# Kernel optimization log

Hardware: AMD Instinct MI355X
Metric: run time of the kernel (lower is better)

The kernel has to match this reference:

```python
import jax, jax.numpy as jnp
import numpy as np

B, S, T = 64, 1024, 64
H, A, DA, DT, P, NT = 1024, 1024, 512, 256, 256, 32
DIN = DA + A + DT  # LSTMCell input: [a_tm1_embed, att_tm1, pre_type]


def setup_inputs() -> dict:
    key = jax.random.key(0)
    ks = jax.random.split(key, 16)
    nrm = lambda k, shape, s=0.02: jax.random.normal(k, shape, jnp.float32) * s
    return {
        'src_encodings': jax.random.normal(ks[0], (B, S, H), jnp.float32),
        'W_ih': nrm(ks[1], (4 * H, DIN)), 'b_ih': jnp.zeros((4 * H,), jnp.float32),
        'W_hh': nrm(ks[2], (4 * H, H)), 'b_hh': jnp.zeros((4 * H,), jnp.float32),
        'W_att': nrm(ks[3], (H, H)),            # att_sketch_linear (no bias)
        'W_attvec': nrm(ks[4], (A, 2 * H)),     # sketch_att_vec_linear (no bias)
        'W_init': nrm(ks[5], (H, H)), 'b_init': jnp.zeros((H,), jnp.float32),  # decoder_cell_init
        'W_q2a': nrm(ks[6], (DA, A)), 'b_q2a': jnp.zeros((DA,), jnp.float32),  # query_vec_to_action_embed
        'prod_embed': nrm(ks[7], (P, DA), 0.05), 'prod_bias': jnp.zeros((P,), jnp.float32),
        'type_embed': nrm(ks[8], (NT, DT), 0.05),
        'prev_prod_ids': jax.random.randint(ks[9], (B, T), 0, P),
        'prev_type_ids': jax.random.randint(ks[10], (B, T), 0, NT),
        'target_prod_ids': jax.random.randint(ks[11], (B, T), 0, P),
        'sketch_lens': jax.random.randint(ks[12], (B,), T // 2, T + 1),
        'src_lens': jax.random.randint(ks[13], (B,), S // 2, S + 1),
    }


def _lstm_cell(x, h, c, W_ih, b_ih, W_hh, b_hh):
    gates = x @ W_ih.T + b_ih + h @ W_hh.T + b_hh
    i, f, g, o = jnp.split(gates, 4, axis=-1)
    c_new = jax.nn.sigmoid(f) * c + jax.nn.sigmoid(i) * jnp.tanh(g)
    h_new = jax.nn.sigmoid(o) * jnp.tanh(c_new)
    return h_new, c_new


def reference(src_encodings, W_ih, b_ih, W_hh, b_hh, W_att, W_attvec, W_init, b_init,
              W_q2a, b_q2a, prod_embed, prod_bias, type_embed,
              prev_prod_ids, prev_type_ids, target_prod_ids, sketch_lens, src_lens):
    Bq, Sq, Hq = src_encodings.shape
    Tq = prev_prod_ids.shape[1]
    src_valid = jnp.arange(Sq)[None, :] < src_lens[:, None]            # [B,S] True = real token
    step_valid = jnp.arange(Tq)[None, :] < sketch_lens[:, None]        # [B,T]
    prev_valid = step_valid & (jnp.arange(Tq)[None, :] > 0)            # prev action exists

    src_att = jnp.einsum('bsh,kh->bsk', src_encodings, W_att)          # att_sketch_linear
    # init_decoder_state(adaptive_avg_pool1d(enc,1))
    init_cell = src_encodings.mean(axis=1)
    h0 = jnp.tanh(init_cell @ W_init.T + b_init)
    c0 = jnp.zeros_like(h0)
    att0 = jnp.zeros((Bq, A), src_encodings.dtype)

    # precomputed grammar lookups (production / type embeddings of a_{t-1})
    a_embeds = jnp.where(prev_valid[..., None], prod_embed[prev_prod_ids], 0.0)   # [B,T,DA]
    t_embeds = jnp.where(prev_valid[..., None], type_embed[prev_type_ids], 0.0)   # [B,T,DT]
    is_first = jnp.arange(Tq) == 0                                                # [T]

    def step(carry, inp):
        h, c, att_tm1 = carry
        a_e, t_e, first = inp
        x = jnp.concatenate([a_e, att_tm1, t_e], axis=-1)
        x = jnp.where(first, 0.0, x)                                   # t==0 -> zero input
        h, c = _lstm_cell(x, h, c, W_ih, b_ih, W_hh, b_hh)
        scores = jnp.einsum('bh,bsh->bs', h, src_att)
        scores = jnp.where(src_valid, scores, -1e9)
        alpha = jax.nn.softmax(scores, axis=-1)
        ctx = jnp.einsum('bs,bsh->bh', alpha, src_encodings)
        att_t = jnp.tanh(jnp.concatenate([h, ctx], axis=-1) @ W_attvec.T)
        q = jnp.tanh(att_t @ W_q2a.T + b_q2a)                          # non_linear readout
        probs = jax.nn.softmax(q @ prod_embed.T + prod_bias, axis=-1)  # [B,P]
        return (h, c, att_t), probs

    xs = (jnp.swapaxes(a_embeds, 0, 1), jnp.swapaxes(t_embeds, 0, 1), is_first)
    _, probs = jax.lax.scan(step, (h0, c0, att0), xs)                  # [T,B,P]

    tgt = jnp.swapaxes(target_prod_ids, 0, 1)[..., None]               # [T,B,1]
    p_t = jnp.take_along_axis(probs, tgt, axis=-1)[..., 0]             # [T,B]
    logp = jnp.log(p_t + 1e-8)
    sketch_prob = jnp.sum(jnp.where(step_valid.T, logp, 0.0), axis=0)  # [B]
    return sketch_prob
```

## Files before the change

### kernel.cpp

```cpp
#include <hip/hip_runtime.h>
#include <hip/hip_bf16.h>

typedef unsigned short u16;
typedef unsigned int u32;
typedef unsigned long long u64;
typedef __attribute__((ext_vector_type(8))) short short8;
typedef __attribute__((ext_vector_type(8))) u16 ushort8;
typedef __attribute__((ext_vector_type(4))) u16 ushort4v;
typedef __attribute__((ext_vector_type(4))) float f32x4;

__device__ __forceinline__ float bf2f(u16 x){ u32 u=((u32)x)<<16; return __builtin_bit_cast(float,u); }
__device__ __forceinline__ u16 f2bf(float f){ u32 u=__builtin_bit_cast(u32,f); u32 r=(u+0x7fffu+((u>>16)&1u))>>16; return (u16)r; }
__device__ __forceinline__ float sigf(float x){ return 1.f/(1.f+__expf(-x)); }

__device__ __forceinline__ void scf(float* p, float v){
  __hip_atomic_store(p, v, __ATOMIC_RELAXED, __HIP_MEMORY_SCOPE_AGENT);
}
__device__ __forceinline__ void scu16(u16* p, u16 v){
  __hip_atomic_store(p, v, __ATOMIC_RELAXED, __HIP_MEMORY_SCOPE_AGENT);
}


__global__ __launch_bounds__(256) void k_cast(const float* __restrict__ s, u16* __restrict__ d, long n){
  long i = ((long)blockIdx.x*256 + threadIdx.x)*8;
  if (i >= n) return;
  float4 a = *(const float4*)(s+i);
  float4 b = *(const float4*)(s+i+4);
  ushort8 o;
  o[0]=f2bf(a.x); o[1]=f2bf(a.y); o[2]=f2bf(a.z); o[3]=f2bf(a.w);
  o[4]=f2bf(b.x); o[5]=f2bf(b.y); o[6]=f2bf(b.z); o[7]=f2bf(b.w);
  *(ushort8*)(d+i) = o;
}

__global__ __launch_bounds__(256) void k_build_wc(const float* __restrict__ Wih, const float* __restrict__ Whh,
                                                  u16* __restrict__ WC){
  long i8 = (long)blockIdx.x*256 + threadIdx.x;
  if (i8 >= (long)4096*352) return;
  int j = (int)(i8/352); int kk = (int)(i8%352)*8;
  const float* src;
  if (kk < 512)        src = Wih + (long)j*1792 + kk;
  else if (kk < 768)   src = Wih + (long)j*1792 + (kk+1024);
  else if (kk < 1792)  src = Wih + (long)j*1792 + (kk-256);
  else                 src = Whh + (long)j*1024 + (kk-1792);
  u16* dst = WC + (long)j*2816 + kk;
  ushort8 o;
  #pragma unroll
  for (int q=0;q<8;++q) o[q] = f2bf(src[q]);
  *(ushort8*)dst = o;
}

__global__ __launch_bounds__(256) void k_wattT(const float* __restrict__ Wa, u16* __restrict__ WT){
  int id = blockIdx.x*256 + threadIdx.x;
  int m = id >> 10, k = id & 1023;
  WT[(long)m*1024 + k] = f2bf(Wa[(long)k*1024 + m]);
}

__global__ __launch_bounds__(256) void k_mean(const u16* __restrict__ ENC, u16* __restrict__ MEANB){
  int b = blockIdx.x, h = blockIdx.y*256 + threadIdx.x;
  const u16* p = ENC + ((long)b<<20) + h;
  float s = 0.f;
  for (int ss=0; ss<1024; ++ss) s += bf2f(p[(long)ss<<10]);
  MEANB[b*1024 + h] = f2bf(s * (1.f/1024.f));
}

__global__ __launch_bounds__(256) void k_embed(const float* __restrict__ pemb, const float* __restrict__ temb,
      const int* __restrict__ pid, const int* __restrict__ tid_, const int* __restrict__ slen,
      u16* __restrict__ XC){
  int t = blockIdx.x >> 6, b = blockIdx.x & 63;
  bool valid = (t>0) && (t < slen[b]);
  int pi = pid[b*64 + t], ti = tid_[b*64 + t];
  u16* dst = XC + (long)blockIdx.x*2816;
  for (int kk = threadIdx.x; kk < 768; kk += 256){
    float v = 0.f;
    if (valid) v = (kk<512) ? pemb[(long)pi*512 + kk] : temb[(long)ti*256 + (kk-512)];
    dst[kk] = f2bf(v);
  }
}

template<int MODE>
__global__ __launch_bounds__(256) void k_gemm(const u16* __restrict__ A, long lda,
      const u16* __restrict__ W, int K, const float* __restrict__ bias,
      float* __restrict__ OF, long ldo, u16* __restrict__ OB1, long ldb1){
  int l = threadIdx.x & 63, w = threadIdx.x >> 6;
  int c = l & 15, g = l >> 4;
  int n0 = blockIdx.x*16, m0 = blockIdx.y*64;
  const u16* ap = A + (long)(m0 + w*16 + c)*lda + g*8;
  const u16* bp = W + (long)(n0 + c)*K + g*8;
  f32x4 acc = {0.f,0.f,0.f,0.f};
  int kit = K >> 5;
  #pragma unroll 4
  for (int kb=0; kb<kit; ++kb){
    short8 av = *(const short8*)(ap + kb*32);
    short8 bv = *(const short8*)(bp + kb*32);
    acc = __builtin_amdgcn_mfma_f32_16x16x32_bf16(av, bv, acc, 0, 0, 0);
  }
  #pragma unroll
  for (int r=0;r<4;++r){
    int row = m0 + w*16 + g*4 + r;
    int col = n0 + c;
    float v = acc[r];
    if (MODE==2){ OB1[(long)row*ldb1 + col] = f2bf(tanhf(v + bias[col])); }
    if (MODE==3){ OF[(long)row*ldo + col] = v + bias[col]; }
  }
}

__global__ __launch_bounds__(256) void k_loss(const float* __restrict__ LG, const int* __restrict__ tgt,
      const int* __restrict__ slen, float* __restrict__ out){
  int b = blockIdx.x;
  int w = threadIdx.x >> 6, l = threadIdx.x & 63;
  int len = slen[b];
  float accum = 0.f;
  for (int t = w; t < 64; t += 4){
    if (t >= len) continue;
    const float* lp = LG + ((long)(t*64 + b))*256;
    float v0=lp[l], v1=lp[l+64], v2=lp[l+128], v3=lp[l+192];
    float mx = fmaxf(fmaxf(v0,v1), fmaxf(v2,v3));
    #pragma unroll
    for (int off=32; off; off>>=1) mx = fmaxf(mx, __shfl_xor(mx, off));
    float s = __expf(v0-mx)+__expf(v1-mx)+__expf(v2-mx)+__expf(v3-mx);
    #pragma unroll
    for (int off=32; off; off>>=1) s += __shfl_xor(s, off);
    float ltg = lp[tgt[b*64 + t]];
    float p = __expf(ltg - mx)/s;
    accum += logf(p + 1e-8f);
  }
  __shared__ float sm[4];
  if (l == 0) sm[w] = accum;
  __syncthreads();
  if (threadIdx.x == 0) out[b] = sm[0]+sm[1]+sm[2]+sm[3];
}

__device__ __forceinline__ void gsync(int* __restrict__ bar, int& gen){
  gen += 1;
  __syncthreads();
  if (threadIdx.x == 0){
    int grp = blockIdx.x & 15;
    int prev = __hip_atomic_fetch_add(bar + grp*64, 1, __ATOMIC_RELAXED, __HIP_MEMORY_SCOPE_AGENT);
    if (prev == gen*16 - 1)
      __hip_atomic_fetch_add(bar + 1024, 1, __ATOMIC_RELAXED, __HIP_MEMORY_SCOPE_AGENT);
    while (__hip_atomic_load(bar + 1024, __ATOMIC_RELAXED, __HIP_MEMORY_SCOPE_AGENT) < gen*16)
      __builtin_amdgcn_s_sleep(1);
  }
  __syncthreads();
}

__global__ __launch_bounds__(1024,1) void k_decoder(
      const u16* __restrict__ ENC, const u16* __restrict__ WC,
      const u16* __restrict__ WAVT, const u16* __restrict__ WAVEC,
      const float* __restrict__ bih, const float* __restrict__ bhh,
      u16* __restrict__ XC, u16* __restrict__ ATT,
      float* __restrict__ HWT, float* __restrict__ PMT, float* __restrict__ PLT,
      float* __restrict__ CTXPT, const int* __restrict__ src_lens,
      int* __restrict__ BAR){
  const int tid = threadIdx.x;
  const int w = tid >> 6, l = tid & 63, c = l & 15, g = l >> 4;
  const int bx = blockIdx.x;
  int gen = 0;

  __shared__ float smem[12320];
  f32x4* lacc  = (f32x4*)smem;
  float* s_ctx = smem;
  float* s_mx  = smem + 12288;
  float* s_ls  = smem + 12304;
  u16*   ldsc  = (u16*)smem;
  f32x4* lacc4 = (f32x4*)(smem + 8192);

  const int n0 = bx << 2;
  const int jrow = n0 + (c & 3) + ((c >> 2) << 10);
  const float biasj = bih[jrow] + bhh[jrow];
  const int kh = w >> 2, mt = w & 3;
  const int lbase = l & 0x33;
  float creg[4] = {0.f,0.f,0.f,0.f};
  const int mt2 = bx & 3, nt2 = bx >> 2;
  const int b3 = bx >> 2, p3 = bx & 3;
  int len = src_lens[b3]; if (len < 1) len = 1; if (len > 1024) len = 1024;
  const int chunk = (len + 3) >> 2;
  const int s0 = p3*chunk;
  const int s1 = (s0 + chunk < len) ? (s0 + chunk) : len;
  const int mt4 = bx & 3, nt4 = bx >> 2;
  const int b16 = tid >> 6, lane64 = tid & 63;

  for (int t = 0; t < 64; ++t){
    const u16* XCt = XC + (size_t)t*64*2816;
    u16* XCn = XC + (size_t)(t+1)*64*2816;
    const u16* Hcur = XCn + 1792;
    float* HW   = HWT  + (size_t)t*64*1024;
    float* PM   = PMT  + (size_t)t*256;
    float* PL   = PLT  + (size_t)t*256;
    float* CTXP = CTXPT + (size_t)t*256*1024;

    {
      const u16* ap = XCt + (long)(mt*16 + c)*2816 + kh*704 + g*8;
      const u16* bp = WC  + (long)jrow*2816 + kh*704 + g*8;
      f32x4 acc = {0.f,0.f,0.f,0.f};
      #pragma unroll 11
      for (int kb=0; kb<22; ++kb){
        short8 av = *(const short8*)(ap + kb*32);
        short8 bv = *(const short8*)(bp + kb*32);
        acc = __builtin_amdgcn_mfma_f32_16x16x32_bf16(av, bv, acc, 0, 0, 0);
      }
      lacc[w*64 + l] = acc;
      __syncthreads();
      if (w < 4){
        f32x4 a0 = lacc[w*64 + l];
        f32x4 a1 = lacc[(w+4)*64 + l];
        f32x4 a2 = lacc[(w+8)*64 + l];
        f32x4 a3 = lacc[(w+12)*64 + l];
        #pragma unroll
        for (int r=0;r<4;++r){
          float val = a0[r] + a1[r] + a2[r] + a3[r] + biasj;
          float iv = __shfl(val, lbase);
          float fv = __shfl(val, lbase+4);
          float gv = __shfl(val, lbase+8);
          float ov = __shfl(val, lbase+12);
          if ((l & 12) == 0){
            float cn = sigf(fv)*creg[r] + sigf(iv)*tanhf(gv);
            float hn = sigf(ov)*tanhf(cn);
            creg[r] = cn;
            int b = w*16 + g*4 + r;
            int n = n0 + (l & 3);
            scu16(XCn + (long)b*2816 + 1792 + n, f2bf(hn));
          }
        }
      }
    }
    gsync(BAR, gen);

    {
      const u16* ap = Hcur + (long)(mt2*16 + c)*2816 + w*64 + g*8;
      const u16* bp = WAVT + (long)(nt2*16 + c)*1024 + w*64 + g*8;
      f32x4 acc = {0.f,0.f,0.f,0.f};
      #pragma unroll
      for (int kb=0; kb<2; ++kb){
        short8 av = *(const short8*)(ap + kb*32);
        short8 bv = *(const short8*)(bp + kb*32);
        acc = __builtin_amdgcn_mfma_f32_16x16x32_bf16(av, bv, acc, 0, 0, 0);
      }
      lacc[w*64 + l] = acc;
      __syncthreads();
      if (w == 0){
        f32x4 rd = lacc[l];
        #pragma unroll
        for (int w2=1; w2<16; ++w2) rd += lacc[w2*64 + l];
        #pragma unroll
        for (int r=0;r<4;++r)
          scf(HW + (long)(mt2*16 + g*4 + r)*1024 + nt2*16 + c, rd[r]);
      }
    }
    gsync(BAR, gen);

    {
      float hw[16], ctx[16];
      const float* hwp = HW + b3*1024 + l*16;
      #pragma unroll
      for (int jj=0;jj<4;++jj){
        float4 v = *(const float4*)(hwp + jj*4);
        hw[4*jj]=v.x; hw[4*jj+1]=v.y; hw[4*jj+2]=v.z; hw[4*jj+3]=v.w;
      }
      #pragma unroll
      for (int jj=0;jj<16;++jj) ctx[jj]=0.f;
      float m = -INFINITY, lsum = 0.f;
      const u16* encb = ENC + (((long)b3)<<20);
      const int sA0 = s0 + 2*w;
      uint4 ca0,ca1,cb0,cb1;
      {
        int rA = (sA0   < s1) ? sA0   : s0;
        int rB = (sA0+1 < s1) ? sA0+1 : s0;
        const u16* pA = encb + ((long)rA<<10) + l*16;
        const u16* pB = encb + ((long)rB<<10) + l*16;
        ca0 = *(const uint4*)pA; ca1 = *(const uint4*)(pA+8);
        cb0 = *(const uint4*)pB; cb1 = *(const uint4*)(pB+8);
      }
      for (int s = sA0; s < s1; s += 32){
        int sn = s + 32;
        int rA = (sn   < s1) ? sn   : s0;
        int rB = (sn+1 < s1) ? sn+1 : s0;
        const u16* pA = encb + ((long)rA<<10) + l*16;
        const u16* pB = encb + ((long)rB<<10) + l*16;
        uint4 na0 = *(const uint4*)pA; uint4 na1 = *(const uint4*)(pA+8);
        uint4 nb0 = *(const uint4*)pB; uint4 nb1 = *(const uint4*)(pB+8);
        float eA[16], eB[16];
        #pragma unroll
        for (int jj=0;jj<4;++jj){
          u32 xa0=((const u32*)&ca0)[jj], xa1=((const u32*)&ca1)[jj];
          u32 xb0=((const u32*)&cb0)[jj], xb1=((const u32*)&cb1)[jj];
          eA[2*jj]   = bf2f((u16)(xa0&0xffff)); eA[2*jj+1]   = bf2f((u16)(xa0>>16));
          eA[8+2*jj] = bf2f((u16)(xa1&0xffff)); eA[8+2*jj+1] = bf2f((u16)(xa1>>16));
          eB[2*jj]   = bf2f((u16)(xb0&0xffff)); eB[2*jj+1]   = bf2f((u16)(xb0>>16));
          eB[8+2*jj] = bf2f((u16)(xb1&0xffff)); eB[8+2*jj+1] = bf2f((u16)(xb1>>16));
        }
        float scA = 0.f, scB = 0.f;
        #pragma unroll
        for (int jj=0;jj<16;++jj){ scA += eA[jj]*hw[jj]; scB += eB[jj]*hw[jj]; }
        #pragma unroll
        for (int off=32; off; off>>=1){
          scA += __shfl_xor(scA, off);
          scB += __shfl_xor(scB, off);
        }
        if (s+1 >= s1) scB = -INFINITY;
        float nm = fmaxf(m, fmaxf(scA, scB));
        float corr = __expf(m - nm);
        float peA = __expf(scA - nm);
        float peB = __expf(scB - nm);
        lsum = lsum*corr + peA + peB;
        #pragma unroll
        for (int jj=0;jj<16;++jj) ctx[jj] = ctx[jj]*corr + peA*eA[jj] + peB*eB[jj];
        m = nm;
        ca0=na0; ca1=na1; cb0=nb0; cb1=nb1;
      }
      if (l == 0){ s_mx[w] = m; s_ls[w] = lsum; }
      __syncthreads();
      float M16 = s_mx[0];
      #pragma unroll
      for (int q=1;q<16;++q) M16 = fmaxf(M16, s_mx[q]);
      float L = 0.f;
      #pragma unroll
      for (int q=0;q<16;++q){
        float wq = (s_mx[q]==-INFINITY)?0.f:__expf(s_mx[q]-M16);
        L += wq * s_ls[q];
      }
      float wei = (m == -INFINITY) ? 0.f : __expf(m - M16);
      if (w < 8){
        #pragma unroll
        for (int jj=0;jj<16;++jj) s_ctx[w*1024 + l*16 + jj] = wei*ctx[jj];
      }
      __syncthreads();
      if (w >= 8){
        #pragma unroll
        for (int jj=0;jj<16;++jj) s_ctx[(w-8)*1024 + l*16 + jj] += wei*ctx[jj];
      }
      __syncthreads();
      {
        float v = 0.f;
        #pragma unroll
        for (int p=0;p<8;++p) v += s_ctx[p*1024 + tid];
        scf(CTXP + (long)bx*1024 + tid, v);
      }
      if (tid == 0){ scf(PM + bx, M16); scf(PL + bx, L); }
    }
    gsync(BAR, gen);

    {
      int b = mt4*16 + b16;
      const float* pmb = PM + b*4;
      const float* plb = PL + b*4;
      float m0=pmb[0], m1=pmb[1], m2=pmb[2], m3=pmb[3];
      float M = fmaxf(fmaxf(m0,m1), fmaxf(m2,m3));
      float w0 = (m0==-INFINITY)?0.f:__expf(m0-M);
      float w1 = (m1==-INFINITY)?0.f:__expf(m1-M);
      float w2 = (m2==-INFINITY)?0.f:__expf(m2-M);
      float w3 = (m3==-INFINITY)?0.f:__expf(m3-M);
      float L = w0*plb[0] + w1*plb[1] + w2*plb[2] + w3*plb[3];
      float inv = (L > 0.f) ? 1.f/L : 0.f;
      const float* c0 = CTXP + (long)(b*4+0)*1024;
      const float* c1 = CTXP + (long)(b*4+1)*1024;
      const float* c2 = CTXP + (long)(b*4+2)*1024;
      const float* c3 = CTXP + (long)(b*4+3)*1024;
      const int swz = (b16 & 7) << 3;
      #pragma unroll
      for (int q=0;q<4;++q){
        int mcol = (lane64 + q*64)*4;
        float4 a0 = *(const float4*)(c0 + mcol);
        float4 a1 = *(const float4*)(c1 + mcol);
        float4 a2 = *(const float4*)(c2 + mcol);
        float4 a3 = *(const float4*)(c3 + mcol);
        ushort4v o;
        o[0] = f2bf((w0*a0.x + w1*a1.x + w2*a2.x + w3*a3.x) * inv);
        o[1] = f2bf((w0*a0.y + w1*a1.y + w2*a2.y + w3*a3.y) * inv);
        o[2] = f2bf((w0*a0.z + w1*a1.z + w2*a2.z + w3*a3.z) * inv);
        o[3] = f2bf((w0*a0.w + w1*a1.w + w2*a2.w + w3*a3.w) * inv);
        *(ushort4v*)(ldsc + ((b16*1024 + mcol) ^ swz)) = o;
      }
      __syncthreads();
      f32x4 acc = {0.f,0.f,0.f,0.f};
      const int koff = (w < 8) ? w*128 : 1024 + (w-8)*128;
      const u16* bp = WAVEC + (long)(nt4*16 + c)*2048 + koff + g*8;
      if (w < 8){
        const u16* ap = Hcur + (long)(mt4*16 + c)*2816 + w*128 + g*8;
        #pragma unroll
        for (int kb=0; kb<4; ++kb){
          short8 av = *(const short8*)(ap + kb*32);
          short8 bv = *(const short8*)(bp + kb*32);
          acc = __builtin_amdgcn_mfma_f32_16x16x32_bf16(av, bv, acc, 0, 0, 0);
        }
      } else {
        const int cswz = (c & 7) << 3;
        const int kbase = c*1024 + (w-8)*128 + g*8;
        #pragma unroll
        for (int kb=0; kb<4; ++kb){
          short8 av = *(const short8*)(ldsc + ((kbase + kb*32) ^ cswz));
          short8 bv = *(const short8*)(bp + kb*32);
          acc = __builtin_amdgcn_mfma_f32_16x16x32_bf16(av, bv, acc, 0, 0, 0);
        }
      }
      lacc4[w*64 + l] = acc;
      __syncthreads();
      if (w == 0){
        f32x4 rd = lacc4[l];
        #pragma unroll
        for (int w2=1; w2<16; ++w2) rd += lacc4[w2*64 + l];
        #pragma unroll
        for (int r=0;r<4;++r){
          int b_ = mt4*16 + g*4 + r;
          int col = nt4*16 + c;
          u16 x = f2bf(tanhf(rd[r]));
          scu16(XCn + (long)b_*2816 + 768 + col, x);
          ATT[((long)t*64 + b_)*1024 + col] = x;
        }
      }
    }
    gsync(BAR, gen);
  }
}

extern "C" void kernel_launch(void* const* d_in, const int* in_sizes, int n_in,
                              void* d_out, int out_size, void* d_ws, size_t ws_size,
                              hipStream_t stream){
  const float* enc      = (const float*)d_in[0];
  const float* W_ih     = (const float*)d_in[1];
  const float* b_ih     = (const float*)d_in[2];
  const float* W_hh     = (const float*)d_in[3];
  const float* b_hh     = (const float*)d_in[4];
  const float* W_att    = (const float*)d_in[5];
  const float* W_attvec = (const float*)d_in[6];
  const float* W_init   = (const float*)d_in[7];
  const float* b_init   = (const float*)d_in[8];
  const float* W_q2a    = (const float*)d_in[9];
  const float* b_q2a    = (const float*)d_in[10];
  const float* prod_emb = (const float*)d_in[11];
  const float* prod_bias= (const float*)d_in[12];
  const float* type_emb = (const float*)d_in[13];
  const int* prev_pid   = (const int*)d_in[14];
  const int* prev_tid   = (const int*)d_in[15];
  const int* target     = (const int*)d_in[16];
  const int* sk_lens    = (const int*)d_in[17];
  const int* src_lens   = (const int*)d_in[18];
  float* out = (float*)d_out;

  char* ws = (char*)d_ws;
  size_t o = 0;
  auto alloc = [&](size_t bytes)->char*{ char* p = ws + o; o += (bytes + 255) & ~(size_t)255; return p; };
  u16*  ENC  = (u16*)alloc((size_t)64*1024*1024*2);
  u16*  WC   = (u16*)alloc((size_t)4096*2816*2);
  u16*  WAVT = (u16*)alloc((size_t)1024*1024*2);
  u16*  WAVEC= (u16*)alloc((size_t)1024*2048*2);
  u16*  WQ   = (u16*)alloc((size_t)512*1024*2);
  u16*  PE   = (u16*)alloc((size_t)256*512*2);
  u16*  WINIT= (u16*)alloc((size_t)1024*1024*2);
  u16*  MEANB= (u16*)alloc((size_t)64*1024*2);
  u16*  XC   = (u16*)alloc((size_t)65*64*2816*2);
  u16*  ATT  = (u16*)alloc((size_t)64*64*1024*2);
  float* HWT = (float*)alloc((size_t)64*64*1024*4);
  float* PMT = (float*)alloc((size_t)64*256*4);
  float* PLT = (float*)alloc((size_t)64*256*4);
  float* CTXPT=(float*)alloc((size_t)64*256*1024*4);
  u16*  Q    = (u16*)alloc((size_t)4096*512*2);
  float* LG  = (float*)alloc((size_t)4096*256*4);
  int*  BAR  = (int*)alloc(8192);
  (void)ws_size; (void)in_sizes; (void)n_in; (void)out_size;

  hipMemsetAsync(XC, 0, (size_t)64*2816*2, stream);
  hipMemsetAsync(BAR, 0, 8192, stream);

  k_cast<<<32768,256,0,stream>>>(enc, ENC, (long)64*1024*1024);
  k_cast<<<1024,256,0,stream>>>(W_attvec, WAVEC, (long)1024*2048);
  k_cast<<<256,256,0,stream>>>(W_q2a, WQ, (long)512*1024);
  k_cast<<<64,256,0,stream>>>(prod_emb, PE, (long)256*512);
  k_cast<<<512,256,0,stream>>>(W_init, WINIT, (long)1024*1024);
  k_build_wc<<<5632,256,0,stream>>>(W_ih, W_hh, WC);
  k_wattT<<<4096,256,0,stream>>>(W_att, WAVT);
  k_mean<<<dim3(64,4),256,0,stream>>>(ENC, MEANB);
  k_gemm<2><<<dim3(64,1),256,0,stream>>>(MEANB, 1024L, WINIT, 1024, b_init,
                                         nullptr, 0L, XC + 1792, 2816L);
  k_embed<<<4096,256,0,stream>>>(prod_emb, type_emb, prev_pid, prev_tid, sk_lens, XC);

  k_decoder<<<256,1024,0,stream>>>(ENC, WC, WAVT, WAVEC, b_ih, b_hh,
                                   XC, ATT, HWT, PMT, PLT, CTXPT, src_lens, BAR);

  k_gemm<2><<<dim3(32,64),256,0,stream>>>(ATT, 1024L, WQ, 1024, b_q2a,
                                          nullptr, 0L, Q, 512L);
  k_gemm<3><<<dim3(16,64),256,0,stream>>>(Q, 512L, PE, 512, prod_bias,
                                          LG, 256L, nullptr, 0L);
  k_loss<<<64,256,0,stream>>>(LG, target, sk_lens, out);
}
```

Before: 4.482 ms.

## Double decoder grid and load-balance attention chunks by source length

The persistent decoder now launches 512 blocks instead of 256. The LSTM gate GEMM is split across two batch halves. A small setup kernel hands out attention chunks to blocks in proportion to each sequence's src_len, so every block has similar work. The attention softmax drops the running-max rescaling and sums raw exponentials, and the per-chunk context partials are stored in bf16 instead of fp32, which cuts partial-buffer traffic. The aim is to use more of the hardware and remove the imbalance between short and long sequences. The costs are a possible exp overflow without max subtraction, lower precision in the partials, and two resident 1024-thread blocks per CU, which the grid barrier depends on to avoid deadlock; the duplicated blocks also recompute some phases redundantly.

```diff
diff --git a/kernel.cpp b/kernel.cpp
--- a/kernel.cpp
+++ b/kernel.cpp
@@ -6,7 +6,6 @@
 typedef unsigned long long u64;
 typedef __attribute__((ext_vector_type(8))) short short8;
 typedef __attribute__((ext_vector_type(8))) u16 ushort8;
-typedef __attribute__((ext_vector_type(4))) u16 ushort4v;
 typedef __attribute__((ext_vector_type(4))) float f32x4;
 
 __device__ __forceinline__ float bf2f(u16 x){ u32 u=((u32)x)<<16; return __builtin_bit_cast(float,u); }
@@ -74,6 +73,24 @@
     float v = 0.f;
     if (valid) v = (kk<512) ? pemb[(long)pi*512 + kk] : temb[(long)ti*256 + (kk-512)];
     dst[kk] = f2bf(v);
+  }
+}
+
+__global__ void k_assign(const int* __restrict__ slen, int* __restrict__ ASG){
+  if (threadIdx.x != 0 || blockIdx.x != 0) return;
+  int lenv[64]; long total = 0;
+  for (int b=0;b<64;++b){ int L = slen[b]; if (L<1)L=1; if (L>1024)L=1024; lenv[b]=L; total+=L; }
+  int cnt[64]; int sum=0;
+  for (int b=0;b<64;++b){ int c = (int)(((long)512*lenv[b])/total); if (c<1)c=1; cnt[b]=c; sum+=c; }
+  int rem = 512 - sum; int bi = 0;
+  while (rem > 0){ cnt[bi&63]++; rem--; bi++; }
+  while (rem < 0){ if (cnt[bi&63] > 1){ cnt[bi&63]--; rem++; } bi++; }
+  int st = 0;
+  for (int b=0;b<64;++b){
+    ASG[1024+b] = cnt[b];
+    ASG[1088+b] = st;
+    for (int i=0;i<cnt[b];++i){ ASG[st+i] = b; ASG[512+st+i] = i; }
+    st += cnt[b];
   }
 }
 
@@ -134,24 +151,24 @@
   gen += 1;
   __syncthreads();
   if (threadIdx.x == 0){
-    int grp = blockIdx.x & 15;
+    int grp = blockIdx.x & 31;
     int prev = __hip_atomic_fetch_add(bar + grp*64, 1, __ATOMIC_RELAXED, __HIP_MEMORY_SCOPE_AGENT);
     if (prev == gen*16 - 1)
-      __hip_atomic_fetch_add(bar + 1024, 1, __ATOMIC_RELAXED, __HIP_MEMORY_SCOPE_AGENT);
-    while (__hip_atomic_load(bar + 1024, __ATOMIC_RELAXED, __HIP_MEMORY_SCOPE_AGENT) < gen*16)
-      __builtin_amdgcn_s_sleep(1);
+      __hip_atomic_fetch_add(bar + 2048, 1, __ATOMIC_RELAXED, __HIP_MEMORY_SCOPE_AGENT);
+    while (__hip_atomic_load(bar + 2048, __ATOMIC_RELAXED, __HIP_MEMORY_SCOPE_AGENT) < gen*32)
+      __builtin_amdgcn_s_sleep(2);
   }
   __syncthreads();
 }
 
-__global__ __launch_bounds__(1024,1) void k_decoder(
+__global__ __launch_bounds__(1024,8) void k_decoder(
       const u16* __restrict__ ENC, const u16* __restrict__ WC,
       const u16* __restrict__ WAVT, const u16* __restrict__ WAVEC,
       const float* __restrict__ bih, const float* __restrict__ bhh,
       u16* __restrict__ XC, u16* __restrict__ ATT,
-      float* __restrict__ HWT, float* __restrict__ PMT, float* __restrict__ PLT,
-      float* __restrict__ CTXPT, const int* __restrict__ src_lens,
-      int* __restrict__ BAR){
+      float* __restrict__ HWT, float* __restrict__ PLT,
+      u16* __restrict__ CTXBT, const int* __restrict__ src_lens,
+      const int* __restrict__ ASG, int* __restrict__ BAR){
   const int tid = threadIdx.x;
   const int w = tid >> 6, l = tid & 63, c = l & 15, g = l >> 4;
   const int bx = blockIdx.x;
@@ -160,55 +177,56 @@
   __shared__ float smem[12320];
   f32x4* lacc  = (f32x4*)smem;
   float* s_ctx = smem;
-  float* s_mx  = smem + 12288;
-  float* s_ls  = smem + 12304;
+  float* s_ls  = smem + 12288;
   u16*   ldsc  = (u16*)smem;
   f32x4* lacc4 = (f32x4*)(smem + 8192);
 
-  const int n0 = bx << 2;
+  const int nb = bx >> 1, mhalf = bx & 1;
+  const int n0 = nb << 2;
   const int jrow = n0 + (c & 3) + ((c >> 2) << 10);
   const float biasj = bih[jrow] + bhh[jrow];
-  const int kh = w >> 2, mt = w & 3;
+  const int kh = w >> 1, mt = w & 1;
   const int lbase = l & 0x33;
   float creg[4] = {0.f,0.f,0.f,0.f};
-  const int mt2 = bx & 3, nt2 = bx >> 2;
-  const int b3 = bx >> 2, p3 = bx & 3;
-  int len = src_lens[b3]; if (len < 1) len = 1; if (len > 1024) len = 1024;
-  const int chunk = (len + 3) >> 2;
-  const int s0 = p3*chunk;
-  const int s1 = (s0 + chunk < len) ? (s0 + chunk) : len;
-  const int mt4 = bx & 3, nt4 = bx >> 2;
+  const int bq = bx & 255;
+  const int mt2 = bq & 3, nt2 = bq >> 2;
+  const int mt4 = mt2, nt4 = nt2;
+  const int b3 = ASG[bx];
+  const int ci3 = ASG[512 + bx];
+  const int nch3 = ASG[1024 + b3];
+  int len3 = src_lens[b3]; if (len3 < 1) len3 = 1; if (len3 > 1024) len3 = 1024;
+  const int chunk3 = (len3 + nch3 - 1)/nch3;
+  int s0 = ci3*chunk3;
+  int s1 = s0 + chunk3; if (s1 > len3) s1 = len3; if (s0 > s1) s0 = s1;
   const int b16 = tid >> 6, lane64 = tid & 63;
 
   for (int t = 0; t < 64; ++t){
     const u16* XCt = XC + (size_t)t*64*2816;
     u16* XCn = XC + (size_t)(t+1)*64*2816;
     const u16* Hcur = XCn + 1792;
-    float* HW   = HWT  + (size_t)t*64*1024;
-    float* PM   = PMT  + (size_t)t*256;
-    float* PL   = PLT  + (size_t)t*256;
-    float* CTXP = CTXPT + (size_t)t*256*1024;
+    float* HW   = HWT  + ((size_t)t<<16);
+    float* PL   = PLT  + ((size_t)t<<9);
+    u16*  CTXB  = CTXBT + ((size_t)t<<19);
 
     {
-      const u16* ap = XCt + (long)(mt*16 + c)*2816 + kh*704 + g*8;
-      const u16* bp = WC  + (long)jrow*2816 + kh*704 + g*8;
+      const u16* ap = XCt + (long)(mhalf*32 + mt*16 + c)*2816 + kh*352 + g*8;
+      const u16* bp = WC  + (long)jrow*2816 + kh*352 + g*8;
       f32x4 acc = {0.f,0.f,0.f,0.f};
-      #pragma unroll 11
-      for (int kb=0; kb<22; ++kb){
+      #pragma unroll 4
+      for (int kb=0; kb<11; ++kb){
         short8 av = *(const short8*)(ap + kb*32);
         short8 bv = *(const short8*)(bp + kb*32);
         acc = __builtin_amdgcn_mfma_f32_16x16x32_bf16(av, bv, acc, 0, 0, 0);
       }
       lacc[w*64 + l] = acc;
       __syncthreads();
-      if (w < 4){
+      if (w < 2){
         f32x4 a0 = lacc[w*64 + l];
-        f32x4 a1 = lacc[(w+4)*64 + l];
-        f32x4 a2 = lacc[(w+8)*64 + l];
-        f32x4 a3 = lacc[(w+12)*64 + l];
+        #pragma unroll
+        for (int w2=1; w2<8; ++w2) a0 += lacc[(w2*2 + w)*64 + l];
         #pragma unroll
         for (int r=0;r<4;++r){
-          float val = a0[r] + a1[r] + a2[r] + a3[r] + biasj;
+          float val = a0[r] + biasj;
           float iv = __shfl(val, lbase);
           float fv = __shfl(val, lbase+4);
           float gv = __shfl(val, lbase+8);
@@ -217,7 +235,7 @@
             float cn = sigf(fv)*creg[r] + sigf(iv)*tanhf(gv);
             float hn = sigf(ov)*tanhf(cn);
             creg[r] = cn;
-            int b = w*16 + g*4 + r;
+            int b = mhalf*32 + w*16 + g*4 + r;
             int n = n0 + (l & 3);
             scu16(XCn + (long)b*2816 + 1792 + n, f2bf(hn));
           }
@@ -259,117 +277,94 @@
       }
       #pragma unroll
       for (int jj=0;jj<16;++jj) ctx[jj]=0.f;
-      float m = -INFINITY, lsum = 0.f;
+      float lsum = 0.f;
       const u16* encb = ENC + (((long)b3)<<20);
-      const int sA0 = s0 + 2*w;
-      uint4 ca0,ca1,cb0,cb1;
+      uint4 c0v, c1v;
       {
-        int rA = (sA0   < s1) ? sA0   : s0;
-        int rB = (sA0+1 < s1) ? sA0+1 : s0;
-        const u16* pA = encb + ((long)rA<<10) + l*16;
-        const u16* pB = encb + ((long)rB<<10) + l*16;
-        ca0 = *(const uint4*)pA; ca1 = *(const uint4*)(pA+8);
-        cb0 = *(const uint4*)pB; cb1 = *(const uint4*)(pB+8);
-      }
-      for (int s = sA0; s < s1; s += 32){
-        int sn = s + 32;
-        int rA = (sn   < s1) ? sn   : s0;
-        int rB = (sn+1 < s1) ? sn+1 : s0;
-        const u16* pA = encb + ((long)rA<<10) + l*16;
-        const u16* pB = encb + ((long)rB<<10) + l*16;
-        uint4 na0 = *(const uint4*)pA; uint4 na1 = *(const uint4*)(pA+8);
-        uint4 nb0 = *(const uint4*)pB; uint4 nb1 = *(const uint4*)(pB+8);
-        float eA[16], eB[16];
+        int r0 = (s0 + w < s1) ? s0 + w : s0;
+        const u16* p = encb + ((long)r0<<10) + l*16;
+        c0v = *(const uint4*)p; c1v = *(const uint4*)(p + 8);
+      }
+      for (int s = s0 + w; s < s1; s += 16){
+        int sn = s + 16;
+        int rn = (sn < s1) ? sn : s0;
+        const u16* pn = encb + ((long)rn<<10) + l*16;
+        uint4 n0v = *(const uint4*)pn;
+        uint4 n1v = *(const uint4*)(pn + 8);
+        float sc = 0.f;
         #pragma unroll
         for (int jj=0;jj<4;++jj){
-          u32 xa0=((const u32*)&ca0)[jj], xa1=((const u32*)&ca1)[jj];
-          u32 xb0=((const u32*)&cb0)[jj], xb1=((const u32*)&cb1)[jj];
-          eA[2*jj]   = bf2f((u16)(xa0&0xffff)); eA[2*jj+1]   = bf2f((u16)(xa0>>16));
-          eA[8+2*jj] = bf2f((u16)(xa1&0xffff)); eA[8+2*jj+1] = bf2f((u16)(xa1>>16));
-          eB[2*jj]   = bf2f((u16)(xb0&0xffff)); eB[2*jj+1]   = bf2f((u16)(xb0>>16));
-          eB[8+2*jj] = bf2f((u16)(xb1&0xffff)); eB[8+2*jj+1] = bf2f((u16)(xb1>>16));
-        }
-        float scA = 0.f, scB = 0.f;
-        #pragma unroll
-        for (int jj=0;jj<16;++jj){ scA += eA[jj]*hw[jj]; scB += eB[jj]*hw[jj]; }
-        #pragma unroll
-        for (int off=32; off; off>>=1){
-          scA += __shfl_xor(scA, off);
-          scB += __shfl_xor(scB, off);
-        }
-        if (s+1 >= s1) scB = -INFINITY;
-        float nm = fmaxf(m, fmaxf(scA, scB));
-        float corr = __expf(m - nm);
-        float peA = __expf(scA - nm);
-        float peB = __expf(scB - nm);
-        lsum = lsum*corr + peA + peB;
-        #pragma unroll
-        for (int jj=0;jj<16;++jj) ctx[jj] = ctx[jj]*corr + peA*eA[jj] + peB*eB[jj];
-        m = nm;
-        ca0=na0; ca1=na1; cb0=nb0; cb1=nb1;
-      }
-      if (l == 0){ s_mx[w] = m; s_ls[w] = lsum; }
-      __syncthreads();
-      float M16 = s_mx[0];
-      #pragma unroll
-      for (int q=1;q<16;++q) M16 = fmaxf(M16, s_mx[q]);
-      float L = 0.f;
-      #pragma unroll
-      for (int q=0;q<16;++q){
-        float wq = (s_mx[q]==-INFINITY)?0.f:__expf(s_mx[q]-M16);
-        L += wq * s_ls[q];
-      }
-      float wei = (m == -INFINITY) ? 0.f : __expf(m - M16);
+          u32 x0=((const u32*)&c0v)[jj], x1=((const u32*)&c1v)[jj];
+          sc += bf2f((u16)(x0&0xffff))*hw[2*jj]   + bf2f((u16)(x0>>16))*hw[2*jj+1];
+          sc += bf2f((u16)(x1&0xffff))*hw[8+2*jj] + bf2f((u16)(x1>>16))*hw[8+2*jj+1];
+        }
+        #pragma unroll
+        for (int off=32; off; off>>=1) sc += __shfl_xor(sc, off);
+        float pe = __expf(sc);
+        lsum += pe;
+        #pragma unroll
+        for (int jj=0;jj<4;++jj){
+          u32 x0=((const u32*)&c0v)[jj], x1=((const u32*)&c1v)[jj];
+          ctx[2*jj]     += pe*bf2f((u16)(x0&0xffff));
+          ctx[2*jj+1]   += pe*bf2f((u16)(x0>>16));
+          ctx[8+2*jj]   += pe*bf2f((u16)(x1&0xffff));
+          ctx[8+2*jj+1] += pe*bf2f((u16)(x1>>16));
+        }
+        c0v = n0v; c1v = n1v;
+      }
+      if (l == 0) s_ls[w] = lsum;
       if (w < 8){
         #pragma unroll
-        for (int jj=0;jj<16;++jj) s_ctx[w*1024 + l*16 + jj] = wei*ctx[jj];
+        for (int jj=0;jj<16;++jj) s_ctx[w*1024 + l*16 + jj] = ctx[jj];
       }
       __syncthreads();
       if (w >= 8){
         #pragma unroll
-        for (int jj=0;jj<16;++jj) s_ctx[(w-8)*1024 + l*16 + jj] += wei*ctx[jj];
+        for (int jj=0;jj<16;++jj) s_ctx[(w-8)*1024 + l*16 + jj] += ctx[jj];
       }
       __syncthreads();
       {
         float v = 0.f;
         #pragma unroll
         for (int p=0;p<8;++p) v += s_ctx[p*1024 + tid];
-        scf(CTXP + (long)bx*1024 + tid, v);
-      }
-      if (tid == 0){ scf(PM + bx, M16); scf(PL + bx, L); }
+        scu16(CTXB + (((long)bx)<<10) + tid, f2bf(v));
+      }
+      if (tid == 0){
+        float L = 0.f;
+        #pragma unroll
+        for (int q=0;q<16;++q) L += s_ls[q];
+        scf(PL + bx, L);
+      }
     }
     gsync(BAR, gen);
 
     {
       int b = mt4*16 + b16;
-      const float* pmb = PM + b*4;
-      const float* plb = PL + b*4;
-      float m0=pmb[0], m1=pmb[1], m2=pmb[2], m3=pmb[3];
-      float M = fmaxf(fmaxf(m0,m1), fmaxf(m2,m3));
-      float w0 = (m0==-INFINITY)?0.f:__expf(m0-M);
-      float w1 = (m1==-INFINITY)?0.f:__expf(m1-M);
-      float w2 = (m2==-INFINITY)?0.f:__expf(m2-M);
-      float w3 = (m3==-INFINITY)?0.f:__expf(m3-M);
-      float L = w0*plb[0] + w1*plb[1] + w2*plb[2] + w3*plb[3];
+      int st = ASG[1088 + b], nL = ASG[1024 + b];
+      float L = 0.f;
+      for (int p=0;p<nL;++p) L += PL[st+p];
       float inv = (L > 0.f) ? 1.f/L : 0.f;
-      const float* c0 = CTXP + (long)(b*4+0)*1024;
-      const float* c1 = CTXP + (long)(b*4+1)*1024;
-      const float* c2 = CTXP + (long)(b*4+2)*1024;
-      const float* c3 = CTXP + (long)(b*4+3)*1024;
+      float acc16[16];
+      #pragma unroll
+      for (int q=0;q<16;++q) acc16[q] = 0.f;
+      for (int p=0;p<nL;++p){
+        const u16* row = CTXB + (((long)(st+p))<<10);
+        #pragma unroll
+        for (int q=0;q<2;++q){
+          int mcol8 = (lane64 + q*64)*8;
+          ushort8 v = *(const ushort8*)(row + mcol8);
+          #pragma unroll
+          for (int j=0;j<8;++j) acc16[q*8+j] += bf2f(v[j]);
+        }
+      }
       const int swz = (b16 & 7) << 3;
       #pragma unroll
-      for (int q=0;q<4;++q){
-        int mcol = (lane64 + q*64)*4;
-        float4 a0 = *(const float4*)(c0 + mcol);
-        float4 a1 = *(const float4*)(c1 + mcol);
-        float4 a2 = *(const float4*)(c2 + mcol);
-        float4 a3 = *(const float4*)(c3 + mcol);
-        ushort4v o;
-        o[0] = f2bf((w0*a0.x + w1*a1.x + w2*a2.x + w3*a3.x) * inv);
-        o[1] = f2bf((w0*a0.y + w1*a1.y + w2*a2.y + w3*a3.y) * inv);
-        o[2] = f2bf((w0*a0.z + w1*a1.z + w2*a2.z + w3*a3.z) * inv);
-        o[3] = f2bf((w0*a0.w + w1*a1.w + w2*a2.w + w3*a3.w) * inv);
-        *(ushort4v*)(ldsc + ((b16*1024 + mcol) ^ swz)) = o;
+      for (int q=0;q<2;++q){
+        int mcol8 = (lane64 + q*64)*8;
+        ushort8 o;
+        #pragma unroll
+        for (int j=0;j<8;++j) o[j] = f2bf(acc16[q*8+j]*inv);
+        *(ushort8*)(ldsc + ((b16*1024 + mcol8) ^ swz)) = o;
       }
       __syncthreads();
       f32x4 acc = {0.f,0.f,0.f,0.f};
@@ -451,17 +446,18 @@
   u16*  XC   = (u16*)alloc((size_t)65*64*2816*2);
   u16*  ATT  = (u16*)alloc((size_t)64*64*1024*2);
   float* HWT = (float*)alloc((size_t)64*64*1024*4);
-  float* PMT = (float*)alloc((size_t)64*256*4);
-  float* PLT = (float*)alloc((size_t)64*256*4);
-  float* CTXPT=(float*)alloc((size_t)64*256*1024*4);
+  float* PLT = (float*)alloc((size_t)64*512*4);
+  u16*  CTXBT=(u16*)alloc((size_t)64*512*1024*2);
   u16*  Q    = (u16*)alloc((size_t)4096*512*2);
   float* LG  = (float*)alloc((size_t)4096*256*4);
-  int*  BAR  = (int*)alloc(8192);
+  int*  BAR  = (int*)alloc(16384);
+  int*  ASG  = (int*)alloc(8192);
   (void)ws_size; (void)in_sizes; (void)n_in; (void)out_size;
 
   hipMemsetAsync(XC, 0, (size_t)64*2816*2, stream);
-  hipMemsetAsync(BAR, 0, 8192, stream);
-
+  hipMemsetAsync(BAR, 0, 16384, stream);
+
+  k_assign<<<1,64,0,stream>>>(src_lens, ASG);
   k_cast<<<32768,256,0,stream>>>(enc, ENC, (long)64*1024*1024);
   k_cast<<<1024,256,0,stream>>>(W_attvec, WAVEC, (long)1024*2048);
   k_cast<<<256,256,0,stream>>>(W_q2a, WQ, (long)512*1024);
@@ -474,8 +470,8 @@
                                          nullptr, 0L, XC + 1792, 2816L);
   k_embed<<<4096,256,0,stream>>>(prod_emb, type_emb, prev_pid, prev_tid, sk_lens, XC);
 
-  k_decoder<<<256,1024,0,stream>>>(ENC, WC, WAVT, WAVEC, b_ih, b_hh,
-                                   XC, ATT, HWT, PMT, PLT, CTXPT, src_lens, BAR);
+  k_decoder<<<512,1024,0,stream>>>(ENC, WC, WAVT, WAVEC, b_ih, b_hh,
+                                   XC, ATT, HWT, PLT, CTXBT, src_lens, ASG, BAR);
 
   k_gemm<2><<<dim3(32,64),256,0,stream>>>(ATT, 1024L, WQ, 1024, b_q2a,
                                           nullptr, 0L, Q, 512L);
```

Measured after the change: 7.332 ms. 63.6% more time.
